# Kernel optimization log

Hardware: AMD Instinct MI355X
Metric: run time of the kernel (lower is better)

Reference implementation:

```python
import jax, jax.numpy as jnp
import numpy as np

NHID = 256
B, T = 128, 2048


def setup_inputs() -> dict:
    key = jax.random.key(0)
    ks = jax.random.split(key, 7)
    s = 1.0 / np.sqrt(NHID)  # torch default uniform bound for RNN/Linear
    u = lambda k, shape, bound: jax.random.uniform(k, shape, jnp.float32, -bound, bound)
    return {
        "x": jax.random.normal(ks[0], (B, T, 1), jnp.float32),
        "W_ih": u(ks[1], (NHID, 1), s),
        "W_hh": u(ks[2], (NHID, NHID), s),
        "b_ih": u(ks[3], (NHID,), s),
        "b_hh": u(ks[4], (NHID,), s),
        "W_out": u(ks[5], (1, NHID), s),
        "b_out": u(ks[6], (1,), s),
    }


def reference(x, W_ih, W_hh, b_ih, b_hh, W_out, b_out):
    # x: [B, T, 1] -> time-major [T, B, 1]
    xt = jnp.transpose(x, (1, 0, 2))
    # Precompute input contribution for all steps: [T, B, H]
    xproj = xt @ W_ih.T + (b_ih + b_hh)

    def step(h, xp):  # h: [B, H], xp: [B, H]
        h_new = jnp.tanh(xp + h @ W_hh.T)
        return h_new, h_new

    h0 = jnp.zeros((x.shape[0], W_hh.shape[0]), dtype=x.dtype)
    _, ys = jax.lax.scan(step, h0, xproj)  # ys: [T, B, H]
    # Output projection then back to batch-major [B, T, 1]
    y = ys @ W_out.T + b_out
    return jnp.transpose(y, (1, 0, 2))
```

## Files before the change

kernel.cpp:

```cpp
#include <hip/hip_runtime.h>
#include <hip/hip_fp16.h>

#define HID  256
#define TT   2048
#define NB   128
#define NTHR 1024

typedef _Float16 hf2 __attribute__((ext_vector_type(2)));

template <int CTRL>
__device__ __forceinline__ float dpp_add(float v) {
    int t = __builtin_amdgcn_update_dpp(0, __float_as_int(v), CTRL, 0xF, 0xF, true);
    return v + __int_as_float(t);
}

__device__ __forceinline__ float tanh_fast(float x) {
    float e = __expf(2.0f * x);
    float r = __builtin_amdgcn_rcpf(e + 1.0f);
    return fmaf(-2.0f, r, 1.0f);
}

__device__ __forceinline__ hf2 bc2(unsigned int u) {
    hf2 h;
    __builtin_memcpy(&h, &u, 4);
    return h;
}

__global__ void pack_w(const float* __restrict__ W, unsigned int* __restrict__ out) {
    int j    = blockIdx.x * 256 + threadIdx.x;
    int k    = j & 3;
    int lane = (j >> 2) & 63;
    int i    = (j >> 8) & 7;
    int wv   = j >> 11;
    int tid  = wv * 64 + lane;
    int row  = 4 * (tid >> 4) + (i >> 1);
    int col  = 16 * (tid & 15) + 8 * (i & 1) + 2 * k;
    _Float16 lo = (_Float16)W[row * HID + col];
    _Float16 hi = (_Float16)W[row * HID + col + 1];
    unsigned short ulo, uhi;
    __builtin_memcpy(&ulo, &lo, 2);
    __builtin_memcpy(&uhi, &hi, 2);
    out[j] = (unsigned int)ulo | ((unsigned int)uhi << 16);
}

#define DOT4(ACC, Tv, Hv) do { \
    ACC = __builtin_amdgcn_fdot2(bc2((Tv).x), bc2((Hv).x), ACC, false); \
    ACC = __builtin_amdgcn_fdot2(bc2((Tv).y), bc2((Hv).y), ACC, false); \
    ACC = __builtin_amdgcn_fdot2(bc2((Tv).z), bc2((Hv).z), ACC, false); \
    ACC = __builtin_amdgcn_fdot2(bc2((Tv).w), bc2((Hv).w), ACC, false); \
} while (0)

#define RED16(A) do { \
    A = dpp_add<0xB1>(A); A = dpp_add<0x4E>(A); \
    A = dpp_add<0x124>(A); A = dpp_add<0x128>(A); \
} while (0)

__global__ __launch_bounds__(NTHR)
void rnn_persist(
    const float* __restrict__ x,
    const float* __restrict__ W_ih,
    const uint4* __restrict__ wq,
    const float* __restrict__ b_ih,
    const float* __restrict__ b_hh,
    const float* __restrict__ W_out,
    const float* __restrict__ b_out,
    float* __restrict__ y)
{
    __shared__ uint4 s_w[4096];
    __shared__ float s_x[TT];
    __shared__ __align__(16) unsigned short s_hh[2][16 * 24];
    __shared__ float s_part[2][16];

    const int tid  = threadIdx.x;
    const int c3   = tid & 15;
    const int rg   = tid >> 4;
    const int lane = tid & 63;
    const int wv   = tid >> 6;
    const int b    = blockIdx.x;

    for (int k = tid; k < TT; k += NTHR) s_x[k] = x[(size_t)b * TT + k];

    for (int j = tid; j < 4096; j += NTHR)
        s_w[j] = wq[j + ((j >> 8) << 8)];

    if (tid < 768) (&s_hh[0][0])[tid] = 0;

    const int   myrow = 4 * rg + (c3 & 3);
    const float wih   = W_ih[myrow];
    const float bias  = b_ih[myrow] + b_hh[myrow];
    const float wo_my = W_out[myrow];
    const float bout  = b_out[0];

    const uint4* lbase = s_w + (wv * 4) * 64 + lane;
    const uint4* sbase = wq + (size_t)(wv * 8 + 4) * 64 + lane;
    const int hwidx  = 24 * (myrow >> 4) + (myrow & 15);
    const int hrbase = 24 * c3;

    __syncthreads();

    int p = 0;
    float* yrow = y + (size_t)b * TT;

    for (int step = 0; step <= TT; ++step) {
        if (step >= 1 && wv == ((step - 1) & 15)) {
            float pp = s_part[(step - 1) & 1][lane & 15];
            pp = dpp_add<0xB1>(pp);
            pp = dpp_add<0x4E>(pp);
            pp = dpp_add<0x124>(pp);
            pp = dpp_add<0x128>(pp);
            if (lane == 0) yrow[step - 1] = pp + bout;
        }
        if (step == TT) break;

        const uint4 T0 = sbase[0];
        const uint4 T1 = sbase[64];
        const uint4 T2 = sbase[128];
        const uint4 T3 = sbase[192];

        const uint4 H0 = *(const uint4*)&s_hh[p][hrbase];
        const uint4 H1 = *(const uint4*)&s_hh[p][hrbase + 8];

        const uint4 L0 = lbase[0];
        const uint4 L1 = lbase[64];
        const uint4 L2 = lbase[128];
        const uint4 L3 = lbase[192];

        const float xt = s_x[step];

        float acc0 = 0.0f, acc1 = 0.0f, acc2 = 0.0f, acc3 = 0.0f;
        DOT4(acc0, L0, H0); DOT4(acc0, L1, H1);
        DOT4(acc1, L2, H0); DOT4(acc1, L3, H1);
        DOT4(acc2, T0, H0); DOT4(acc2, T1, H1);
        DOT4(acc3, T2, H0); DOT4(acc3, T3, H1);

        RED16(acc0); RED16(acc1); RED16(acc2); RED16(acc3);

        float s01 = (c3 & 1) ? acc1 : acc0;
        float s23 = (c3 & 1) ? acc3 : acc2;
        float dot = (c3 & 2) ? s23 : s01;
        float hn  = tanh_fast(fmaf(xt, wih, bias) + dot);

        if ((c3 & 12) == 0) {
            _Float16 hh = (_Float16)hn;
            unsigned short us;
            __builtin_memcpy(&us, &hh, 2);
            s_hh[p ^ 1][hwidx] = us;
        }

        float pv = ((c3 & 12) == 0) ? hn * wo_my : 0.0f;
        pv = dpp_add<0xB1>(pv);
        pv = dpp_add<0x4E>(pv);
        pv = dpp_add<0x124>(pv);
        pv = dpp_add<0x128>(pv);
        pv = dpp_add<0x142>(pv);
        pv = dpp_add<0x143>(pv);
        if (lane == 63) s_part[step & 1][wv] = pv;

        __syncthreads();
        p ^= 1;
    }
}

extern "C" void kernel_launch(void* const* d_in, const int* in_sizes, int n_in,
                              void* d_out, int out_size, void* d_ws, size_t ws_size,
                              hipStream_t stream) {
    const float* x     = (const float*)d_in[0];
    const float* W_ih  = (const float*)d_in[1];
    const float* W_hh  = (const float*)d_in[2];
    const float* b_ih  = (const float*)d_in[3];
    const float* b_hh  = (const float*)d_in[4];
    const float* W_out = (const float*)d_in[5];
    const float* b_out = (const float*)d_in[6];
    float* y = (float*)d_out;
    unsigned int* wpk = (unsigned int*)d_ws;

    hipLaunchKernelGGL(pack_w, dim3(128), dim3(256), 0, stream, W_hh, wpk);
    hipLaunchKernelGGL(rnn_persist, dim3(NB), dim3(NTHR), 0, stream,
                       x, W_ih, (const uint4*)wpk, b_ih, b_hh, W_out, b_out, y);
}
```

Baseline: 1.478 ms.

## Move more weights to global with inline-asm software prefetch across steps

Shrinks the LDS-resident weight slice from half to a quarter of each wave's W_hh fragment and loads the remaining three quarters from global/L2 with inline-asm global_load_dwordx4. Those loads are issued one step ahead so their latency overlaps the reduction, tanh and barrier of the current step. A dummy 40KB shared pad, touched only under an impossible branch, is added to keep LDS usage high, apparently to hold occupancy or placement at one block per CU. The trade is more global/L2 traffic per step and a forced vmcnt(0) wait, in exchange for fewer LDS reads and hidden load latency.

Result: slower. 1.887 ms (+27.7%).

```diff
diff --git a/kernel.cpp b/kernel.cpp
--- a/kernel.cpp
+++ b/kernel.cpp
@@ -7,6 +7,7 @@
 #define NTHR 1024
 
 typedef _Float16 hf2 __attribute__((ext_vector_type(2)));
+typedef unsigned int u32x4 __attribute__((ext_vector_type(4)));
 
 template <int CTRL>
 __device__ __forceinline__ float dpp_add(float v) {
@@ -43,11 +44,20 @@
     out[j] = (unsigned int)ulo | ((unsigned int)uhi << 16);
 }
 
+#define GLOAD(dst, ptr, OFF) \
+    asm volatile("global_load_dwordx4 %0, %1, off offset:" #OFF \
+                 : "=&v"(dst) : "v"(ptr))
+
+#define PREFETCH() do { \
+    GLOAD(U2, pA, 0); GLOAD(U3, pA, 1024); GLOAD(U4, pA, 2048); \
+    GLOAD(U5, pB, 0); GLOAD(U6, pB, 1024); GLOAD(U7, pB, 2048); \
+} while (0)
+
 #define DOT4(ACC, Tv, Hv) do { \
-    ACC = __builtin_amdgcn_fdot2(bc2((Tv).x), bc2((Hv).x), ACC, false); \
-    ACC = __builtin_amdgcn_fdot2(bc2((Tv).y), bc2((Hv).y), ACC, false); \
-    ACC = __builtin_amdgcn_fdot2(bc2((Tv).z), bc2((Hv).z), ACC, false); \
-    ACC = __builtin_amdgcn_fdot2(bc2((Tv).w), bc2((Hv).w), ACC, false); \
+    ACC = __builtin_amdgcn_fdot2(bc2((Tv)[0]), bc2((Hv)[0]), ACC, false); \
+    ACC = __builtin_amdgcn_fdot2(bc2((Tv)[1]), bc2((Hv)[1]), ACC, false); \
+    ACC = __builtin_amdgcn_fdot2(bc2((Tv)[2]), bc2((Hv)[2]), ACC, false); \
+    ACC = __builtin_amdgcn_fdot2(bc2((Tv)[3]), bc2((Hv)[3]), ACC, false); \
 } while (0)
 
 #define RED16(A) do { \
@@ -59,17 +69,18 @@
 void rnn_persist(
     const float* __restrict__ x,
     const float* __restrict__ W_ih,
-    const uint4* __restrict__ wq,
+    const u32x4* __restrict__ wq,
     const float* __restrict__ b_ih,
     const float* __restrict__ b_hh,
     const float* __restrict__ W_out,
     const float* __restrict__ b_out,
     float* __restrict__ y)
 {
-    __shared__ uint4 s_w[4096];
+    __shared__ u32x4 s_w[2048];
     __shared__ float s_x[TT];
     __shared__ __align__(16) unsigned short s_hh[2][16 * 24];
     __shared__ float s_part[2][16];
+    __shared__ float s_pad[10240];
 
     const int tid  = threadIdx.x;
     const int c3   = tid & 15;
@@ -78,10 +89,16 @@
     const int wv   = tid >> 6;
     const int b    = blockIdx.x;
 
+    if (b == -1) {
+        volatile float* vp = s_pad;
+        vp[tid] = 1.0f;
+        y[tid] = vp[tid];
+    }
+
     for (int k = tid; k < TT; k += NTHR) s_x[k] = x[(size_t)b * TT + k];
 
-    for (int j = tid; j < 4096; j += NTHR)
-        s_w[j] = wq[j + ((j >> 8) << 8)];
+    for (int j = tid; j < 2048; j += NTHR)
+        s_w[j] = wq[((j >> 7) * 8 + ((j >> 6) & 1)) * 64 + (j & 63)];
 
     if (tid < 768) (&s_hh[0][0])[tid] = 0;
 
@@ -91,10 +108,14 @@
     const float wo_my = W_out[myrow];
     const float bout  = b_out[0];
 
-    const uint4* lbase = s_w + (wv * 4) * 64 + lane;
-    const uint4* sbase = wq + (size_t)(wv * 8 + 4) * 64 + lane;
+    const u32x4* lbase = s_w + (wv * 2) * 64 + lane;
+    const u32x4* pA = wq + (size_t)(wv * 8 + 2) * 64 + lane;
+    const u32x4* pB = wq + (size_t)(wv * 8 + 5) * 64 + lane;
     const int hwidx  = 24 * (myrow >> 4) + (myrow & 15);
     const int hrbase = 24 * c3;
+
+    u32x4 U2, U3, U4, U5, U6, U7;
+    PREFETCH();
 
     __syncthreads();
 
@@ -112,26 +133,23 @@
         }
         if (step == TT) break;
 
-        const uint4 T0 = sbase[0];
-        const uint4 T1 = sbase[64];
-        const uint4 T2 = sbase[128];
-        const uint4 T3 = sbase[192];
-
-        const uint4 H0 = *(const uint4*)&s_hh[p][hrbase];
-        const uint4 H1 = *(const uint4*)&s_hh[p][hrbase + 8];
-
-        const uint4 L0 = lbase[0];
-        const uint4 L1 = lbase[64];
-        const uint4 L2 = lbase[128];
-        const uint4 L3 = lbase[192];
+        const u32x4 H0 = *(const u32x4*)&s_hh[p][hrbase];
+        const u32x4 H1 = *(const u32x4*)&s_hh[p][hrbase + 8];
+        const u32x4 L0 = lbase[0];
+        const u32x4 L1 = lbase[64];
 
         const float xt = s_x[step];
 
         float acc0 = 0.0f, acc1 = 0.0f, acc2 = 0.0f, acc3 = 0.0f;
         DOT4(acc0, L0, H0); DOT4(acc0, L1, H1);
-        DOT4(acc1, L2, H0); DOT4(acc1, L3, H1);
-        DOT4(acc2, T0, H0); DOT4(acc2, T1, H1);
-        DOT4(acc3, T2, H0); DOT4(acc3, T3, H1);
+
+        asm volatile("s_waitcnt vmcnt(0)" ::: "memory");
+        __builtin_amdgcn_sched_barrier(0);
+        DOT4(acc1, U2, H0); DOT4(acc1, U3, H1);
+        DOT4(acc2, U4, H0); DOT4(acc2, U5, H1);
+        DOT4(acc3, U6, H0); DOT4(acc3, U7, H1);
+
+        PREFETCH();
 
         RED16(acc0); RED16(acc1); RED16(acc2); RED16(acc3);
 
@@ -176,5 +194,5 @@
 
     hipLaunchKernelGGL(pack_w, dim3(128), dim3(256), 0, stream, W_hh, wpk);
     hipLaunchKernelGGL(rnn_persist, dim3(NB), dim3(NTHR), 0, stream,
-                       x, W_ih, (const uint4*)wpk, b_ih, b_hh, W_out, b_out, y);
+                       x, W_ih, (const u32x4*)wpk, b_ih, b_hh, W_out, b_out, y);
 }
```
